# Performance work log

Hardware: AMD Instinct MI355X
Metric: run time of the kernel (lower is better)

## Reference

```python
import jax, jax.numpy as jnp
import numpy as np

B, T, J, D = 64, 2048, 128, 512


def setup_inputs() -> dict:
    key = jax.random.key(0)
    k1, k2, k3, k4 = jax.random.split(key, 4)
    question = jax.random.normal(k1, (B, J, D), dtype=jnp.float32)
    context = jax.random.normal(k2, (B, T, D), dtype=jnp.float32)
    question_len = jax.random.randint(k3, (B,), 1, J + 1, dtype=jnp.int32)
    context_len = jax.random.randint(k4, (B,), 1, T + 1, dtype=jnp.int32)
    weight = jnp.ones((D, 1), dtype=jnp.float32)  # initializer='ones'
    return {"question": question, "context": context,
            "question_len": question_len, "context_len": context_len,
            "weight": weight}


def reference(question, context, question_len, context_len, weight):
    # Original computes sum_d context[b,t,d]*question[b,j,d]*w[d] via a
    # broadcast [B,T,J,D] intermediate; reformulated as a batched GEMM.
    w = weight[:, 0]                                   # [D]
    sim = jnp.einsum('btd,bjd->btj', context * w, question)  # [B,T,J]
    Jm = question.shape[1]
    Tm = context.shape[1]
    q_mask = (jnp.arange(Jm) < question_len[:, None]).astype(jnp.float32)  # [B,J]
    c_mask = (jnp.arange(Tm) < context_len[:, None]).astype(jnp.float32)   # [B,T]
    mask = c_mask[:, :, None] * q_mask[:, None, :]     # [B,T,J]
    neg = jnp.finfo(jnp.float32).min
    sim = sim + neg * (1.0 - mask)
    attn = jax.nn.softmax(sim, axis=1)                 # softmax over context axis T
    return jnp.sum(attn * mask, axis=2)[..., None]     # [B,T,1]
```

## Files before the change

### kernel.cpp

```cpp
#include <hip/hip_runtime.h>
#include <stdint.h>
#include <math.h>

#define BB 64
#define TT 2048
#define JJ 128
#define DD 512
#define BK 32

typedef short short8 __attribute__((ext_vector_type(8)));
typedef float f32x4 __attribute__((ext_vector_type(4)));

__device__ inline unsigned pk_hi(float a, float b) {
  return __builtin_amdgcn_perm(__float_as_uint(b), __float_as_uint(a), 0x07060302u);
}
__device__ inline float truncbf(float x) {
  return __uint_as_float(__float_as_uint(x) & 0xFFFF0000u);
}
__device__ inline void pack8(float4 a, float4 b, uint4& h, uint4& l) {
  h = make_uint4(pk_hi(a.x, a.y), pk_hi(a.z, a.w), pk_hi(b.x, b.y), pk_hi(b.z, b.w));
  float l0 = a.x - truncbf(a.x), l1 = a.y - truncbf(a.y);
  float l2 = a.z - truncbf(a.z), l3 = a.w - truncbf(a.w);
  float l4 = b.x - truncbf(b.x), l5 = b.y - truncbf(b.y);
  float l6 = b.z - truncbf(b.z), l7 = b.w - truncbf(b.w);
  l = make_uint4(pk_hi(l0, l1), pk_hi(l2, l3), pk_hi(l4, l5), pk_hi(l6, l7));
}
__device__ inline short8 bc8(uint4 u) { return __builtin_bit_cast(short8, u); }

__global__ __launch_bounds__(256)
void qpack_kernel(const float* __restrict__ Qm, const float* __restrict__ w,
                  uint4* __restrict__ Qhi, uint4* __restrict__ Qlo) {
  const int gid = blockIdx.x * 256 + threadIdx.x;
  const int lane = gid & 63;
  const int mi = (gid >> 6) & 3;
  const int str = (gid >> 8) & 1;
  const int ks = (gid >> 9) & 15;
  const int b = gid >> 13;
  const int j = str * 64 + mi * 16 + (lane & 15);
  const int c = lane >> 4;

  const float* qp = Qm + ((size_t)b * JJ + j) * DD + ks * BK + c * 8;
  const float* wp = w + ks * BK + c * 8;
  float4 a = *(const float4*)qp;
  float4 bq = *(const float4*)(qp + 4);
  float4 wa = *(const float4*)wp;
  float4 wb = *(const float4*)(wp + 4);
  a.x *= wa.x; a.y *= wa.y; a.z *= wa.z; a.w *= wa.w;
  bq.x *= wb.x; bq.y *= wb.y; bq.z *= wb.z; bq.w *= wb.w;
  uint4 h, l;
  pack8(a, bq, h, l);
  Qhi[gid] = h;
  Qlo[gid] = l;
}

__global__ __launch_bounds__(256, 1)
void sim_gemm_mfma(const uint4* __restrict__ Qhi, const uint4* __restrict__ Qlo,
                   const float* __restrict__ Cm, const int* __restrict__ qlen,
                   const int* __restrict__ clen, float* __restrict__ S) {
  const int id = blockIdx.x;
  const int nid = (id & 7) * 128 + (id >> 3);
  const int b = nid >> 4;
  const int t0 = (nid & 15) * 128;

  const int cl = clen[b];
  if (t0 >= cl) return;
  const int ql = qlen[b];

  const int tid = threadIdx.x;
  const int lane = tid & 63;
  const int wv = tid >> 6;
  const int wm = (wv & 1) * 64;
  const int wn = (wv >> 1) * 64;
  const int l15 = lane & 15;
  const int q = lane >> 4;

  bool mact[4];
#pragma unroll
  for (int i = 0; i < 4; i++) mact[i] = (wm + i * 16) < ql;
  if (!mact[0]) return;

  const uint4* ahp = Qhi + (size_t)b * 8192 + (wv & 1) * 256 + lane;
  const uint4* alp = Qlo + (size_t)b * 8192 + (wv & 1) * 256 + lane;
  const float* cb = Cm + ((size_t)b * TT + t0 + wn + l15) * DD + q * 8;

  f32x4 acc[4][4] = {};

  for (int ks = 0; ks < 16; ks++) {
    float4 cv0[4], cv1[4];
#pragma unroll
    for (int ni = 0; ni < 4; ni++) {
      const float* cp = cb + ni * 16 * DD + ks * BK;
      cv0[ni] = *(const float4*)cp;
      cv1[ni] = *(const float4*)(cp + 4);
    }
    uint4 ahv[4], alv[4];
#pragma unroll
    for (int mi = 0; mi < 4; mi++) {
      if (mact[mi]) {
        ahv[mi] = ahp[ks * 512 + mi * 64];
        alv[mi] = alp[ks * 512 + mi * 64];
      }
    }
    short8 bh[4], bl[4];
#pragma unroll
    for (int ni = 0; ni < 4; ni++) {
      uint4 h, l;
      pack8(cv0[ni], cv1[ni], h, l);
      bh[ni] = bc8(h);
      bl[ni] = bc8(l);
    }
#pragma unroll
    for (int mi = 0; mi < 4; mi++) {
      if (!mact[mi]) continue;
      short8 ah = bc8(ahv[mi]);
      short8 al = bc8(alv[mi]);
#pragma unroll
      for (int ni = 0; ni < 4; ni++) {
        acc[mi][ni] = __builtin_amdgcn_mfma_f32_16x16x32_bf16(ah, bh[ni], acc[mi][ni], 0, 0, 0);
        acc[mi][ni] = __builtin_amdgcn_mfma_f32_16x16x32_bf16(al, bh[ni], acc[mi][ni], 0, 0, 0);
        acc[mi][ni] = __builtin_amdgcn_mfma_f32_16x16x32_bf16(ah, bl[ni], acc[mi][ni], 0, 0, 0);
      }
    }
  }

#pragma unroll
  for (int mi = 0; mi < 4; mi++) {
    if (!mact[mi]) continue;
#pragma unroll
    for (int ni = 0; ni < 4; ni++) {
      const int j = wm + mi * 16 + q * 4;
      const int t = t0 + wn + ni * 16 + l15;
      float* dst = S + ((size_t)b * JJ + j) * TT + t;
      dst[0 * TT] = acc[mi][ni][0];
      dst[1 * TT] = acc[mi][ni][1];
      dst[2 * TT] = acc[mi][ni][2];
      dst[3 * TT] = acc[mi][ni][3];
    }
  }
}

__global__ __launch_bounds__(256)
void softmax_stats_kernel(const float* __restrict__ S, const int* __restrict__ qlen,
                          const int* __restrict__ clen, float* __restrict__ m_out,
                          float* __restrict__ r_out) {
  const int j = blockIdx.x;
  const int b = blockIdx.y;
  if (j >= qlen[b]) return;
  const int cl = clen[b];
  const int tid = threadIdx.x;
  const float4* row = (const float4*)(S + ((size_t)b * JJ + j) * TT);

  const float NEG = -3.4e38f;
  float4 v0 = make_float4(NEG, NEG, NEG, NEG);
  float4 v1 = make_float4(NEG, NEG, NEG, NEG);
  const int t0 = tid * 4;
  const int t1 = (tid + 256) * 4;
  if (t0 < cl) v0 = row[tid];
  if (t1 < cl) v1 = row[tid + 256];

  float m = NEG;
  m = fmaxf(m, (t0 + 0 < cl) ? v0.x : NEG);
  m = fmaxf(m, (t0 + 1 < cl) ? v0.y : NEG);
  m = fmaxf(m, (t0 + 2 < cl) ? v0.z : NEG);
  m = fmaxf(m, (t0 + 3 < cl) ? v0.w : NEG);
  m = fmaxf(m, (t1 + 0 < cl) ? v1.x : NEG);
  m = fmaxf(m, (t1 + 1 < cl) ? v1.y : NEG);
  m = fmaxf(m, (t1 + 2 < cl) ? v1.z : NEG);
  m = fmaxf(m, (t1 + 3 < cl) ? v1.w : NEG);

  __shared__ float red[8];
#pragma unroll
  for (int off = 32; off > 0; off >>= 1) m = fmaxf(m, __shfl_down(m, off));
  if ((tid & 63) == 0) red[tid >> 6] = m;
  __syncthreads();
  m = fmaxf(fmaxf(red[0], red[1]), fmaxf(red[2], red[3]));

  float s = 0.f;
  s += (t0 + 0 < cl) ? __expf(v0.x - m) : 0.f;
  s += (t0 + 1 < cl) ? __expf(v0.y - m) : 0.f;
  s += (t0 + 2 < cl) ? __expf(v0.z - m) : 0.f;
  s += (t0 + 3 < cl) ? __expf(v0.w - m) : 0.f;
  s += (t1 + 0 < cl) ? __expf(v1.x - m) : 0.f;
  s += (t1 + 1 < cl) ? __expf(v1.y - m) : 0.f;
  s += (t1 + 2 < cl) ? __expf(v1.z - m) : 0.f;
  s += (t1 + 3 < cl) ? __expf(v1.w - m) : 0.f;
#pragma unroll
  for (int off = 32; off > 0; off >>= 1) s += __shfl_down(s, off);
  if ((tid & 63) == 0) red[4 + (tid >> 6)] = s;
  __syncthreads();
  s = red[4] + red[5] + red[6] + red[7];

  if (tid == 0) {
    m_out[(size_t)b * JJ + j] = m;
    r_out[(size_t)b * JJ + j] = 1.f / s;
  }
}

__global__ __launch_bounds__(256)
void out_kernel(const float* __restrict__ S, const float* __restrict__ m_arr,
                const float* __restrict__ r_arr, const int* __restrict__ qlen,
                const int* __restrict__ clen, float* __restrict__ out) {
  const int b = blockIdx.y;
  const int t = blockIdx.x * 256 + threadIdx.x;
  const int ql = qlen[b];
  const int cl = clen[b];

  __shared__ float lm[JJ];
  __shared__ float lr[JJ];
  if (threadIdx.x < ql) {
    lm[threadIdx.x] = m_arr[(size_t)b * JJ + threadIdx.x];
    lr[threadIdx.x] = r_arr[(size_t)b * JJ + threadIdx.x];
  }
  __syncthreads();

  float acc = 0.f;
  if (t < cl) {
    const float* col = S + (size_t)b * JJ * TT + t;
#pragma unroll 4
    for (int j = 0; j < ql; j++) {
      acc += __expf(col[(size_t)j * TT] - lm[j]) * lr[j];
    }
  }
  out[(size_t)b * TT + t] = acc;
}

extern "C" void kernel_launch(void* const* d_in, const int* in_sizes, int n_in,
                              void* d_out, int out_size, void* d_ws, size_t ws_size,
                              hipStream_t stream) {
  const float* question = (const float*)d_in[0];
  const float* context  = (const float*)d_in[1];
  const int*   qlen     = (const int*)d_in[2];
  const int*   clen     = (const int*)d_in[3];
  const float* weight   = (const float*)d_in[4];
  float* out = (float*)d_out;

  float* S = (float*)d_ws;
  float* m_arr = S + (size_t)BB * JJ * TT;
  float* r_arr = m_arr + (size_t)BB * JJ;
  uint4* Qhi = (uint4*)(r_arr + (size_t)BB * JJ);
  uint4* Qlo = Qhi + (size_t)BB * 16 * 512;

  qpack_kernel<<<dim3(2048), 256, 0, stream>>>(question, weight, Qhi, Qlo);
  sim_gemm_mfma<<<dim3(1024), 256, 0, stream>>>(Qhi, Qlo, context, qlen, clen, S);
  softmax_stats_kernel<<<dim3(JJ, BB), 256, 0, stream>>>(S, qlen, clen, m_arr, r_arr);
  out_kernel<<<dim3(TT / 256, BB), 256, 0, stream>>>(S, m_arr, r_arr, qlen, clen, out);
}
```

Before: 397.6 us.

## Fuse question bf16 split-packing into GEMM and prefetch context tiles

Removes the separate qpack kernel. The GEMM now loads raw fp32 question rows, applies the weight and splits them into hi/lo bf16 inside the k-loop. It also adds register double-buffering of the context loads for the next k-step and raises launch bounds to allow two blocks per CU. This saves one launch and the packed-Q round trip through memory, but redoes the weight multiply and packing for every t-tile and adds register pressure.

```diff
diff --git a/kernel.cpp b/kernel.cpp
--- a/kernel.cpp
+++ b/kernel.cpp
@@ -27,34 +27,8 @@
 }
 __device__ inline short8 bc8(uint4 u) { return __builtin_bit_cast(short8, u); }
 
-__global__ __launch_bounds__(256)
-void qpack_kernel(const float* __restrict__ Qm, const float* __restrict__ w,
-                  uint4* __restrict__ Qhi, uint4* __restrict__ Qlo) {
-  const int gid = blockIdx.x * 256 + threadIdx.x;
-  const int lane = gid & 63;
-  const int mi = (gid >> 6) & 3;
-  const int str = (gid >> 8) & 1;
-  const int ks = (gid >> 9) & 15;
-  const int b = gid >> 13;
-  const int j = str * 64 + mi * 16 + (lane & 15);
-  const int c = lane >> 4;
-
-  const float* qp = Qm + ((size_t)b * JJ + j) * DD + ks * BK + c * 8;
-  const float* wp = w + ks * BK + c * 8;
-  float4 a = *(const float4*)qp;
-  float4 bq = *(const float4*)(qp + 4);
-  float4 wa = *(const float4*)wp;
-  float4 wb = *(const float4*)(wp + 4);
-  a.x *= wa.x; a.y *= wa.y; a.z *= wa.z; a.w *= wa.w;
-  bq.x *= wb.x; bq.y *= wb.y; bq.z *= wb.z; bq.w *= wb.w;
-  uint4 h, l;
-  pack8(a, bq, h, l);
-  Qhi[gid] = h;
-  Qlo[gid] = l;
-}
-
-__global__ __launch_bounds__(256, 1)
-void sim_gemm_mfma(const uint4* __restrict__ Qhi, const uint4* __restrict__ Qlo,
+__global__ __launch_bounds__(256, 2)
+void sim_gemm_mfma(const float* __restrict__ Qm, const float* __restrict__ w,
                    const float* __restrict__ Cm, const int* __restrict__ qlen,
                    const int* __restrict__ clen, float* __restrict__ S) {
   const int id = blockIdx.x;
@@ -79,27 +53,51 @@
   for (int i = 0; i < 4; i++) mact[i] = (wm + i * 16) < ql;
   if (!mact[0]) return;
 
-  const uint4* ahp = Qhi + (size_t)b * 8192 + (wv & 1) * 256 + lane;
-  const uint4* alp = Qlo + (size_t)b * 8192 + (wv & 1) * 256 + lane;
-  const float* cb = Cm + ((size_t)b * TT + t0 + wn + l15) * DD + q * 8;
+  const float* qa[4];
+#pragma unroll
+  for (int mi = 0; mi < 4; mi++)
+    qa[mi] = Qm + ((size_t)b * JJ + wm + mi * 16 + l15) * DD + q * 8;
+  const float* ca[4];
+#pragma unroll
+  for (int ni = 0; ni < 4; ni++)
+    ca[ni] = Cm + ((size_t)b * TT + t0 + wn + ni * 16 + l15) * DD + q * 8;
+  const float* wp = w + q * 8;
 
   f32x4 acc[4][4] = {};
 
+  float4 pb0[4], pb1[4];
+#pragma unroll
+  for (int ni = 0; ni < 4; ni++) {
+    pb0[ni] = *(const float4*)(ca[ni]);
+    pb1[ni] = *(const float4*)(ca[ni] + 4);
+  }
+
+#pragma unroll 1
   for (int ks = 0; ks < 16; ks++) {
     float4 cv0[4], cv1[4];
 #pragma unroll
-    for (int ni = 0; ni < 4; ni++) {
-      const float* cp = cb + ni * 16 * DD + ks * BK;
-      cv0[ni] = *(const float4*)cp;
-      cv1[ni] = *(const float4*)(cp + 4);
-    }
-    uint4 ahv[4], alv[4];
+    for (int ni = 0; ni < 4; ni++) { cv0[ni] = pb0[ni]; cv1[ni] = pb1[ni]; }
+    if (ks < 15) {
+#pragma unroll
+      for (int ni = 0; ni < 4; ni++) {
+        pb0[ni] = *(const float4*)(ca[ni] + (ks + 1) * BK);
+        pb1[ni] = *(const float4*)(ca[ni] + (ks + 1) * BK + 4);
+      }
+    }
+    const float4 w0 = *(const float4*)(wp + ks * BK);
+    const float4 w1 = *(const float4*)(wp + ks * BK + 4);
+    short8 ah[4], al[4];
 #pragma unroll
     for (int mi = 0; mi < 4; mi++) {
-      if (mact[mi]) {
-        ahv[mi] = ahp[ks * 512 + mi * 64];
-        alv[mi] = alp[ks * 512 + mi * 64];
-      }
+      if (!mact[mi]) continue;
+      float4 a0 = *(const float4*)(qa[mi] + ks * BK);
+      float4 a1 = *(const float4*)(qa[mi] + ks * BK + 4);
+      a0.x *= w0.x; a0.y *= w0.y; a0.z *= w0.z; a0.w *= w0.w;
+      a1.x *= w1.x; a1.y *= w1.y; a1.z *= w1.z; a1.w *= w1.w;
+      uint4 h, l;
+      pack8(a0, a1, h, l);
+      ah[mi] = bc8(h);
+      al[mi] = bc8(l);
     }
     short8 bh[4], bl[4];
 #pragma unroll
@@ -112,13 +110,11 @@
 #pragma unroll
     for (int mi = 0; mi < 4; mi++) {
       if (!mact[mi]) continue;
-      short8 ah = bc8(ahv[mi]);
-      short8 al = bc8(alv[mi]);
 #pragma unroll
       for (int ni = 0; ni < 4; ni++) {
-        acc[mi][ni] = __builtin_amdgcn_mfma_f32_16x16x32_bf16(ah, bh[ni], acc[mi][ni], 0, 0, 0);
-        acc[mi][ni] = __builtin_amdgcn_mfma_f32_16x16x32_bf16(al, bh[ni], acc[mi][ni], 0, 0, 0);
-        acc[mi][ni] = __builtin_amdgcn_mfma_f32_16x16x32_bf16(ah, bl[ni], acc[mi][ni], 0, 0, 0);
+        acc[mi][ni] = __builtin_amdgcn_mfma_f32_16x16x32_bf16(ah[mi], bh[ni], acc[mi][ni], 0, 0, 0);
+        acc[mi][ni] = __builtin_amdgcn_mfma_f32_16x16x32_bf16(al[mi], bh[ni], acc[mi][ni], 0, 0, 0);
+        acc[mi][ni] = __builtin_amdgcn_mfma_f32_16x16x32_bf16(ah[mi], bl[ni], acc[mi][ni], 0, 0, 0);
       }
     }
   }
@@ -237,11 +233,8 @@
   float* S = (float*)d_ws;
   float* m_arr = S + (size_t)BB * JJ * TT;
   float* r_arr = m_arr + (size_t)BB * JJ;
-  uint4* Qhi = (uint4*)(r_arr + (size_t)BB * JJ);
-  uint4* Qlo = Qhi + (size_t)BB * 16 * 512;
-
-  qpack_kernel<<<dim3(2048), 256, 0, stream>>>(question, weight, Qhi, Qlo);
-  sim_gemm_mfma<<<dim3(1024), 256, 0, stream>>>(Qhi, Qlo, context, qlen, clen, S);
+
+  sim_gemm_mfma<<<dim3(1024), 256, 0, stream>>>(question, weight, context, qlen, clen, S);
   softmax_stats_kernel<<<dim3(JJ, BB), 256, 0, stream>>>(S, qlen, clen, m_arr, r_arr);
   out_kernel<<<dim3(TT / 256, BB), 256, 0, stream>>>(S, m_arr, r_arr, qlen, clen, out);
 }
```

After: 432.1 us. 1.09x slower.
